# Optimization experiments

Measured on AMD Instinct MI355X. Metric: run time of the kernel, lower is better.

Reference implementation:

```python
import jax, jax.numpy as jnp
import numpy as np

B, A, C, H, W = 2, 4, 3, 32, 32
N = H * W * A  # 4096 proposals
EPS = 1e-6


def setup_inputs() -> dict:
    key = jax.random.key(0)
    k1, k2, k3, k4 = jax.random.split(key, 4)
    scores = jax.random.normal(k1, (B, A * C, H, W), jnp.float32)
    bbox_preds = jax.random.normal(k2, (B, A * 7, H, W), jnp.float32)
    pp_params = jax.random.normal(k3, (B, C * 3, H, W), jnp.float32)
    # decoded LiDAR boxes (x, y, z, dx, dy, dz, yaw) with positive sizes
    u = jax.random.uniform(k4, (B, N, 7), jnp.float32)
    scale = jnp.array([80.0, 80.0, 4.0, 4.0, 4.0, 3.0, 6.28], jnp.float32)
    shift = jnp.array([-40.0, -40.0, -2.0, 0.5, 0.5, 0.5, -3.14], jnp.float32)
    decoded = u * scale + shift
    return {"scores": scores, "bbox_preds": bbox_preds,
            "pp_params": pp_params, "decoded": decoded}


def _nearest_bev(dec):
    # dec: [B, N, 7] -> axis-aligned nearest BEV boxes [B, N, 4] (x1,y1,x2,y2)
    bev = dec[..., jnp.array([0, 1, 3, 4, 6])]  # x, y, dx, dy, yaw
    rot = bev[..., 4]
    period = jnp.pi
    # limit_period(rot, offset=0.5, period=pi)
    normed = jnp.abs(rot - jnp.floor(rot / period + 0.5) * period)
    cond = (normed > jnp.pi / 4)[..., None]
    xywh = jnp.where(cond, bev[..., jnp.array([0, 1, 3, 2])], bev[..., :4])
    ctr, dims = xywh[..., :2], xywh[..., 2:]
    return jnp.concatenate([ctr - dims / 2, ctr + dims / 2], axis=-1)


def _pairwise_iou(boxes):
    # boxes: [B, N, 4] -> iou [B, N, N]
    lt = jnp.maximum(boxes[:, :, None, :2], boxes[:, None, :, :2])
    rb = jnp.minimum(boxes[:, :, None, 2:], boxes[:, None, :, 2:])
    wh = jnp.clip(rb - lt, 0.0)
    inter = wh[..., 0] * wh[..., 1]
    area = (boxes[..., 2] - boxes[..., 0]) * (boxes[..., 3] - boxes[..., 1])
    union = area[:, :, None] + area[:, None, :] - inter
    return inter / jnp.maximum(union, EPS)


def _forward_scores(scores, pp_params, decoded):
    # flatten scores: [B, A*C, H, W] -> [B, N, C]
    sc = scores.reshape(B, A, C, H, W).transpose(0, 3, 4, 1, 2).reshape(B, N, C)
    # flatten pp: [B, C*3, H, W] -> [B, H, W, C, 3] -> expand over A -> [B, N, C, 3]
    pp = pp_params.reshape(B, C, 3, H, W).transpose(0, 3, 4, 1, 2)
    pp = jnp.broadcast_to(pp[:, :, :, None], (B, H, W, A, C, 3)).reshape(B, N, C, 3)

    iou = _pairwise_iou(_nearest_bev(decoded[..., :7]))  # [B, N, N]
    sm_sc = jax.nn.softmax(sc, axis=1)  # softmax over proposal dim per class

    per_class = []
    for c in range(C):  # C is small and fixed
        p0 = pp[:, :, c, 0]
        p1 = pp[:, :, c, 1]
        weight = jax.nn.softmax(iou + p0[:, :, None] * p1[:, None, :], axis=2)
        per_class.append(jnp.einsum('bij,bj->bi', weight, sm_sc[:, :, c]))
    new_sc = jnp.stack(per_class, axis=-1)  # [B, N, C]

    # back to level layout: [B, N, C] -> [B, A*C, H, W]
    return new_sc.reshape(B, H, W, A, C).transpose(0, 3, 4, 1, 2).reshape(B, A * C, H, W)


def reference(scores, bbox_preds, pp_params, decoded):
    out_scores = _forward_scores(scores, pp_params, decoded)
    # original returns (out_scores_list, bbox_preds, dir_cls, pp_params); dir_cls=None
    return out_scores, bbox_preds, pp_params
```

## Files before the change

kernel.cpp:

```cpp
#include <hip/hip_runtime.h>
#include <math.h>

#define B_   2
#define C_   3
#define HW_  1024
#define N_   4096
#define AC_  12

#define PI_F    3.14159265358979323846f
#define L2E     1.4426950408889634f
#define INV_L2E 0.6931471805599453f

#define OUT0_ELEMS 24576
#define OUT1_ELEMS 57344
#define OUT2_ELEMS 18432

#define ROWBLK   16
#define JTILE    512
#define NTILE    8
#define MAINBLKS 512
#define CPBLKS   32
#define CP_F4_BBOX 14336
#define CP_F4_TOT  18944

#if __has_builtin(__builtin_amdgcn_exp2f)
#define EXP2F(x) __builtin_amdgcn_exp2f(x)
#else
#define EXP2F(x) __expf((x) * INV_L2E)
#endif

__device__ __forceinline__ float4 make_box(const float* __restrict__ d) {
    float x = d[0], y = d[1], d3 = d[3], d4 = d[4], rot = d[6];
    float kq = floorf(rot / PI_F + 0.5f);
    float normed = fabsf(rot - kq * PI_F);
    bool swap_wh = normed > (0.25f * PI_F);
    float w = swap_wh ? d4 : d3;
    float h = swap_wh ? d3 : d4;
    return make_float4(x - 0.5f * w, y - 0.5f * h, x + 0.5f * w, y + 0.5f * h);
}

__global__ __launch_bounds__(512) void k_fused(
    const float* __restrict__ scores, const float* __restrict__ pp,
    const float* __restrict__ dec, const float* __restrict__ bbox,
    float* __restrict__ out)
{
    const int blk = blockIdx.x;
    const int t = threadIdx.x;

    if (blk >= MAINBLKS) {
        const float4* src1 = (const float4*)bbox;
        const float4* src2 = (const float4*)pp;
        float4* dst1 = (float4*)(out + OUT0_ELEMS);
        float4* dst2 = (float4*)(out + OUT0_ELEMS + OUT1_ELEMS);
        for (int u = (blk - MAINBLKS) * 512 + t; u < CP_F4_TOT;
             u += CPBLKS * 512) {
            if (u < CP_F4_BBOX) dst1[u] = src1[u];
            else                dst2[u - CP_F4_BBOX] = src2[u - CP_F4_BBOX];
        }
        return;
    }

    const int b = blk >> 8;
    const int rowblk = blk & 255;
    const int r = t & 15;
    const int q = t >> 4;

    const float* __restrict__ decb = dec + b * (N_ * 7);
    const float* __restrict__ scb  = scores + b * (AC_ * HW_);
    const float* __restrict__ ppb  = pp + b * (9 * HW_);

    __shared__ float4 s_box[JTILE];
    __shared__ float4 s_aux[JTILE];
    __shared__ float4 s_p1[JTILE];
    __shared__ float2 s_red[8][ROWBLK][C_];
    __shared__ float  s_Sp[8][C_];

    const int i0 = rowblk * ROWBLK + r;
    const float4 bx0 = make_box(decb + i0 * 7);
    const float ar0 = (bx0.z - bx0.x) * (bx0.w - bx0.y) * INV_L2E;
    const int hw0 = i0 >> 2;
    const float p00x = ppb[0 * HW_ + hw0] * L2E;
    const float p00y = ppb[3 * HW_ + hw0] * L2E;
    const float p00z = ppb[6 * HW_ + hw0] * L2E;

    float n00 = 0.f, d00 = 0.f, n01 = 0.f, d01 = 0.f, n02 = 0.f, d02 = 0.f;
    float sS0 = 0.f, sS1 = 0.f, sS2 = 0.f;

    float ld0, ld1, ld3, ld4, ld6, ls0, ls1, ls2, lp1a, lp1b, lp1c;
    {
        const float* dj = decb + t * 7;
        ld0 = dj[0]; ld1 = dj[1]; ld3 = dj[3]; ld4 = dj[4]; ld6 = dj[6];
        const int hw = t >> 2, a = t & 3;
        ls0 = scb[(a * C_ + 0) * HW_ + hw];
        ls1 = scb[(a * C_ + 1) * HW_ + hw];
        ls2 = scb[(a * C_ + 2) * HW_ + hw];
        lp1a = ppb[1 * HW_ + hw]; lp1b = ppb[4 * HW_ + hw]; lp1c = ppb[7 * HW_ + hw];
    }

    for (int tile = 0; tile < NTILE; ++tile) {
        if (tile) __syncthreads();
        {
            float kq = floorf(ld6 / PI_F + 0.5f);
            float normed = fabsf(ld6 - kq * PI_F);
            bool sw = normed > (0.25f * PI_F);
            float w = sw ? ld4 : ld3, h = sw ? ld3 : ld4;
            float4 box = make_float4(ld0 - 0.5f * w, ld1 - 0.5f * h,
                                     ld0 + 0.5f * w, ld1 + 0.5f * h);
            float area = (box.z - box.x) * (box.w - box.y);
            float e0 = __expf(ls0), e1 = __expf(ls1), e2 = __expf(ls2);
            sS0 += e0; sS1 += e1; sS2 += e2;
            s_box[t] = box;
            s_aux[t] = make_float4(area * INV_L2E, e0, e1, e2);
            s_p1[t]  = make_float4(lp1a, lp1b, lp1c, 0.f);
        }
        __syncthreads();
        if (tile + 1 < NTILE) {
            const int j = (tile + 1) * JTILE + t;
            const float* dj = decb + j * 7;
            ld0 = dj[0]; ld1 = dj[1]; ld3 = dj[3]; ld4 = dj[4]; ld6 = dj[6];
            const int hw = j >> 2, a = j & 3;
            ls0 = scb[(a * C_ + 0) * HW_ + hw];
            ls1 = scb[(a * C_ + 1) * HW_ + hw];
            ls2 = scb[(a * C_ + 2) * HW_ + hw];
            lp1a = ppb[1 * HW_ + hw]; lp1b = ppb[4 * HW_ + hw]; lp1c = ppb[7 * HW_ + hw];
        }
#pragma unroll 4
        for (int m = 0; m < 16; ++m) {
            const int jj = q + (m << 5);
            const float4 bj = s_box[jj];
            const float4 ax = s_aux[jj];
            const float4 pj = s_p1[jj];
            float x1 = fmaxf(bx0.x, bj.x), y1 = fmaxf(bx0.y, bj.y);
            float x2 = fminf(bx0.z, bj.z), y2 = fminf(bx0.w, bj.w);
            float w = fmaxf(x2 - x1, 0.f), h = fmaxf(y2 - y1, 0.f);
            float inter = w * h;
            float uni = fmaf(inter, -INV_L2E, ar0 + ax.x);
            float iou = inter * __builtin_amdgcn_rcpf(uni);
            float e0 = EXP2F(fmaf(p00x, pj.x, iou));
            float e1 = EXP2F(fmaf(p00y, pj.y, iou));
            float e2 = EXP2F(fmaf(p00z, pj.z, iou));
            n00 = fmaf(e0, ax.y, n00); d00 += e0;
            n01 = fmaf(e1, ax.z, n01); d01 += e1;
            n02 = fmaf(e2, ax.w, n02); d02 += e2;
        }
    }

#define RED4(v) { v += __shfl_xor(v, 16); v += __shfl_xor(v, 32); }
    RED4(n00) RED4(d00) RED4(n01) RED4(d01) RED4(n02) RED4(d02)
#undef RED4
    const int wv = t >> 6, lane = t & 63;
    if (lane < ROWBLK) {
        s_red[wv][lane][0] = make_float2(n00, d00);
        s_red[wv][lane][1] = make_float2(n01, d01);
        s_red[wv][lane][2] = make_float2(n02, d02);
    }
#pragma unroll
    for (int off = 1; off < 64; off <<= 1) {
        sS0 += __shfl_xor(sS0, off);
        sS1 += __shfl_xor(sS1, off);
        sS2 += __shfl_xor(sS2, off);
    }
    if (lane == 0) { s_Sp[wv][0] = sS0; s_Sp[wv][1] = sS1; s_Sp[wv][2] = sS2; }
    __syncthreads();

    if (t < C_ * ROWBLK) {
        const int c = t >> 4, row = t & 15;
        float num = 0.f, den = 0.f, S = 0.f;
#pragma unroll
        for (int w = 0; w < 8; ++w) {
            float2 v = s_red[w][row][c];
            num += v.x; den += v.y;
            S += s_Sp[w][c];
        }
        const int n = rowblk * ROWBLK + row;
        out[(b * AC_ + (n & 3) * C_ + c) * HW_ + (n >> 2)] = num / (den * S);
    }
}

extern "C" void kernel_launch(void* const* d_in, const int* in_sizes, int n_in,
                              void* d_out, int out_size, void* d_ws, size_t ws_size,
                              hipStream_t stream) {
    (void)d_ws; (void)ws_size;
    const float* scores = (const float*)d_in[0];
    const float* bbox   = (const float*)d_in[1];
    const float* pp     = (const float*)d_in[2];
    const float* dec    = (const float*)d_in[3];
    k_fused<<<MAINBLKS + CPBLKS, 512, 0, stream>>>(
        scores, pp, dec, bbox, (float*)d_out);
}
```

Before: 93.97 us.

## Register-block four rows per thread and double-buffer shared tiles

Each thread now handles four consecutive rows (the four anchors that share one hw position and its pp values), so every column entry read from shared memory is reused four times. The shared staging arrays are double-buffered, which allows the next tile to be written while the current one is consumed and removes one barrier per tile. Launch bounds now request 4 blocks per CU. The change cuts LDS traffic and barriers but raises register pressure and lengthens the shuffle reduction.

Measured after the change: 96.97 us. +3.2%, slower.

```diff
diff --git a/kernel.cpp b/kernel.cpp
--- a/kernel.cpp
+++ b/kernel.cpp
@@ -16,6 +16,7 @@
 #define OUT2_ELEMS 18432
 
 #define ROWBLK   16
+#define RPT      4
 #define JTILE    512
 #define NTILE    8
 #define MAINBLKS 512
@@ -39,7 +40,7 @@
     return make_float4(x - 0.5f * w, y - 0.5f * h, x + 0.5f * w, y + 0.5f * h);
 }
 
-__global__ __launch_bounds__(512) void k_fused(
+__global__ __launch_bounds__(512, 4) void k_fused(
     const float* __restrict__ scores, const float* __restrict__ pp,
     const float* __restrict__ dec, const float* __restrict__ bbox,
     float* __restrict__ out)
@@ -62,31 +63,36 @@
 
     const int b = blk >> 8;
     const int rowblk = blk & 255;
-    const int r = t & 15;
-    const int q = t >> 4;
+    const int r = t & 3;
+    const int q = t >> 2;
 
     const float* __restrict__ decb = dec + b * (N_ * 7);
     const float* __restrict__ scb  = scores + b * (AC_ * HW_);
     const float* __restrict__ ppb  = pp + b * (9 * HW_);
 
-    __shared__ float4 s_box[JTILE];
-    __shared__ float4 s_aux[JTILE];
-    __shared__ float4 s_p1[JTILE];
+    __shared__ float4 s_box[2][JTILE];
+    __shared__ float4 s_aux[2][JTILE];
+    __shared__ float4 s_p1 [2][JTILE];
     __shared__ float2 s_red[8][ROWBLK][C_];
     __shared__ float  s_Sp[8][C_];
 
-    const int i0 = rowblk * ROWBLK + r;
-    const float4 bx0 = make_box(decb + i0 * 7);
-    const float ar0 = (bx0.z - bx0.x) * (bx0.w - bx0.y) * INV_L2E;
+    const int i0 = rowblk * ROWBLK + (r << 2);
     const int hw0 = i0 >> 2;
-    const float p00x = ppb[0 * HW_ + hw0] * L2E;
-    const float p00y = ppb[3 * HW_ + hw0] * L2E;
-    const float p00z = ppb[6 * HW_ + hw0] * L2E;
-
-    float n00 = 0.f, d00 = 0.f, n01 = 0.f, d01 = 0.f, n02 = 0.f, d02 = 0.f;
+    float4 bx[RPT]; float ar[RPT];
+#pragma unroll
+    for (int k = 0; k < RPT; ++k) {
+        bx[k] = make_box(decb + (i0 + k) * 7);
+        ar[k] = (bx[k].z - bx[k].x) * (bx[k].w - bx[k].y) * INV_L2E;
+    }
+    const float p0x = ppb[0 * HW_ + hw0] * L2E;
+    const float p0y = ppb[3 * HW_ + hw0] * L2E;
+    const float p0z = ppb[6 * HW_ + hw0] * L2E;
+
+    float accn[RPT][C_] = {}, accd[RPT][C_] = {};
     float sS0 = 0.f, sS1 = 0.f, sS2 = 0.f;
 
     float ld0, ld1, ld3, ld4, ld6, ls0, ls1, ls2, lp1a, lp1b, lp1c;
+
     {
         const float* dj = decb + t * 7;
         ld0 = dj[0]; ld1 = dj[1]; ld3 = dj[3]; ld4 = dj[4]; ld6 = dj[6];
@@ -95,25 +101,24 @@
         ls1 = scb[(a * C_ + 1) * HW_ + hw];
         ls2 = scb[(a * C_ + 2) * HW_ + hw];
         lp1a = ppb[1 * HW_ + hw]; lp1b = ppb[4 * HW_ + hw]; lp1c = ppb[7 * HW_ + hw];
-    }
-
+        float kq = floorf(ld6 / PI_F + 0.5f);
+        float nr = fabsf(ld6 - kq * PI_F);
+        bool sw = nr > (0.25f * PI_F);
+        float w = sw ? ld4 : ld3, h = sw ? ld3 : ld4;
+        float4 box = make_float4(ld0 - 0.5f * w, ld1 - 0.5f * h,
+                                 ld0 + 0.5f * w, ld1 + 0.5f * h);
+        float area = (box.z - box.x) * (box.w - box.y);
+        float e0 = __expf(ls0), e1 = __expf(ls1), e2 = __expf(ls2);
+        sS0 += e0; sS1 += e1; sS2 += e2;
+        s_box[0][t] = box;
+        s_aux[0][t] = make_float4(area * INV_L2E, e0, e1, e2);
+        s_p1 [0][t] = make_float4(lp1a, lp1b, lp1c, 0.f);
+    }
+    __syncthreads();
+
+#pragma unroll 1
     for (int tile = 0; tile < NTILE; ++tile) {
-        if (tile) __syncthreads();
-        {
-            float kq = floorf(ld6 / PI_F + 0.5f);
-            float normed = fabsf(ld6 - kq * PI_F);
-            bool sw = normed > (0.25f * PI_F);
-            float w = sw ? ld4 : ld3, h = sw ? ld3 : ld4;
-            float4 box = make_float4(ld0 - 0.5f * w, ld1 - 0.5f * h,
-                                     ld0 + 0.5f * w, ld1 + 0.5f * h);
-            float area = (box.z - box.x) * (box.w - box.y);
-            float e0 = __expf(ls0), e1 = __expf(ls1), e2 = __expf(ls2);
-            sS0 += e0; sS1 += e1; sS2 += e2;
-            s_box[t] = box;
-            s_aux[t] = make_float4(area * INV_L2E, e0, e1, e2);
-            s_p1[t]  = make_float4(lp1a, lp1b, lp1c, 0.f);
-        }
-        __syncthreads();
+        const int cur = tile & 1;
         if (tile + 1 < NTILE) {
             const int j = (tile + 1) * JTILE + t;
             const float* dj = decb + j * 7;
@@ -124,35 +129,65 @@
             ls2 = scb[(a * C_ + 2) * HW_ + hw];
             lp1a = ppb[1 * HW_ + hw]; lp1b = ppb[4 * HW_ + hw]; lp1c = ppb[7 * HW_ + hw];
         }
-#pragma unroll 4
-        for (int m = 0; m < 16; ++m) {
-            const int jj = q + (m << 5);
-            const float4 bj = s_box[jj];
-            const float4 ax = s_aux[jj];
-            const float4 pj = s_p1[jj];
-            float x1 = fmaxf(bx0.x, bj.x), y1 = fmaxf(bx0.y, bj.y);
-            float x2 = fminf(bx0.z, bj.z), y2 = fminf(bx0.w, bj.w);
-            float w = fmaxf(x2 - x1, 0.f), h = fmaxf(y2 - y1, 0.f);
-            float inter = w * h;
-            float uni = fmaf(inter, -INV_L2E, ar0 + ax.x);
-            float iou = inter * __builtin_amdgcn_rcpf(uni);
-            float e0 = EXP2F(fmaf(p00x, pj.x, iou));
-            float e1 = EXP2F(fmaf(p00y, pj.y, iou));
-            float e2 = EXP2F(fmaf(p00z, pj.z, iou));
-            n00 = fmaf(e0, ax.y, n00); d00 += e0;
-            n01 = fmaf(e1, ax.z, n01); d01 += e1;
-            n02 = fmaf(e2, ax.w, n02); d02 += e2;
-        }
-    }
-
-#define RED4(v) { v += __shfl_xor(v, 16); v += __shfl_xor(v, 32); }
-    RED4(n00) RED4(d00) RED4(n01) RED4(d01) RED4(n02) RED4(d02)
-#undef RED4
+#pragma unroll 2
+        for (int m = 0; m < JTILE / 128; ++m) {
+            const int jj = q + (m << 7);
+            const float4 bj = s_box[cur][jj];
+            const float4 ax = s_aux[cur][jj];
+            const float4 pj = s_p1 [cur][jj];
+#pragma unroll
+            for (int k = 0; k < RPT; ++k) {
+                float x1 = fmaxf(bx[k].x, bj.x), y1 = fmaxf(bx[k].y, bj.y);
+                float x2 = fminf(bx[k].z, bj.z), y2 = fminf(bx[k].w, bj.w);
+                float w = fmaxf(x2 - x1, 0.f), h = fmaxf(y2 - y1, 0.f);
+                float inter = w * h;
+                float uni = fmaf(inter, -INV_L2E, ar[k] + ax.x);
+                float iou = inter * __builtin_amdgcn_rcpf(uni);
+                float e0 = EXP2F(fmaf(p0x, pj.x, iou));
+                float e1 = EXP2F(fmaf(p0y, pj.y, iou));
+                float e2 = EXP2F(fmaf(p0z, pj.z, iou));
+                accn[k][0] = fmaf(e0, ax.y, accn[k][0]); accd[k][0] += e0;
+                accn[k][1] = fmaf(e1, ax.z, accn[k][1]); accd[k][1] += e1;
+                accn[k][2] = fmaf(e2, ax.w, accn[k][2]); accd[k][2] += e2;
+            }
+        }
+        if (tile + 1 < NTILE) {
+            float kq = floorf(ld6 / PI_F + 0.5f);
+            float nr = fabsf(ld6 - kq * PI_F);
+            bool sw = nr > (0.25f * PI_F);
+            float w = sw ? ld4 : ld3, h = sw ? ld3 : ld4;
+            float4 box = make_float4(ld0 - 0.5f * w, ld1 - 0.5f * h,
+                                     ld0 + 0.5f * w, ld1 + 0.5f * h);
+            float area = (box.z - box.x) * (box.w - box.y);
+            float e0 = __expf(ls0), e1 = __expf(ls1), e2 = __expf(ls2);
+            sS0 += e0; sS1 += e1; sS2 += e2;
+            const int nxt = cur ^ 1;
+            s_box[nxt][t] = box;
+            s_aux[nxt][t] = make_float4(area * INV_L2E, e0, e1, e2);
+            s_p1 [nxt][t] = make_float4(lp1a, lp1b, lp1c, 0.f);
+        }
+        __syncthreads();
+    }
+
+#pragma unroll
+    for (int k = 0; k < RPT; ++k)
+#pragma unroll
+        for (int c = 0; c < C_; ++c) {
+            float nv = accn[k][c], dv = accd[k][c];
+            nv += __shfl_xor(nv, 4);  dv += __shfl_xor(dv, 4);
+            nv += __shfl_xor(nv, 8);  dv += __shfl_xor(dv, 8);
+            nv += __shfl_xor(nv, 16); dv += __shfl_xor(dv, 16);
+            nv += __shfl_xor(nv, 32); dv += __shfl_xor(dv, 32);
+            accn[k][c] = nv; accd[k][c] = dv;
+        }
     const int wv = t >> 6, lane = t & 63;
-    if (lane < ROWBLK) {
-        s_red[wv][lane][0] = make_float2(n00, d00);
-        s_red[wv][lane][1] = make_float2(n01, d01);
-        s_red[wv][lane][2] = make_float2(n02, d02);
+    if (lane < 4) {
+#pragma unroll
+        for (int k = 0; k < RPT; ++k)
+#pragma unroll
+            for (int c = 0; c < C_; ++c)
+                s_red[wv][(lane << 2) + k][c] =
+                    make_float2(accn[k][c], accd[k][c]);
     }
 #pragma unroll
     for (int off = 1; off < 64; off <<= 1) {
```

## Factor pp term out of exp across anchor groups and compute two rows per thread

Applied to the files above, without the earlier changes.

Splits exp(iou + p0*p1) into exp(iou)*exp(p0*p1). The p1 value is shared by the 4 anchors at each spatial location, so the per-class exp is computed once per location rather than once per proposal, and only one exp(iou) is needed per pair instead of three. Each thread now handles two rows, sharing the shared-memory loads of column boxes and halving the number of blocks, which lowers parallelism. The factored exponentials can overflow or lose precision if the two terms are large with opposite signs.

Measured after the change: 85.64 us. 8.9% less time.

```diff
diff --git a/kernel.cpp b/kernel.cpp
--- a/kernel.cpp
+++ b/kernel.cpp
@@ -15,10 +15,11 @@
 #define OUT1_ELEMS 57344
 #define OUT2_ELEMS 18432
 
-#define ROWBLK   16
+#define ROWBLK   32
 #define JTILE    512
+#define QTILE    128
 #define NTILE    8
-#define MAINBLKS 512
+#define MAINBLKS 256
 #define CPBLKS   32
 #define CP_F4_BBOX 14336
 #define CP_F4_TOT  18944
@@ -60,8 +61,8 @@
         return;
     }
 
-    const int b = blk >> 8;
-    const int rowblk = blk & 255;
+    const int b = blk >> 7;
+    const int rowblk = blk & 127;
     const int r = t & 15;
     const int q = t >> 4;
 
@@ -71,22 +72,24 @@
 
     __shared__ float4 s_box[JTILE];
     __shared__ float4 s_aux[JTILE];
-    __shared__ float4 s_p1[JTILE];
+    __shared__ float4 s_p1q[QTILE];
     __shared__ float2 s_red[8][ROWBLK][C_];
     __shared__ float  s_Sp[8][C_];
 
-    const int i0 = rowblk * ROWBLK + r;
+    const int i0 = rowblk * ROWBLK + (r << 1);
     const float4 bx0 = make_box(decb + i0 * 7);
+    const float4 bx1 = make_box(decb + (i0 + 1) * 7);
     const float ar0 = (bx0.z - bx0.x) * (bx0.w - bx0.y) * INV_L2E;
+    const float ar1 = (bx1.z - bx1.x) * (bx1.w - bx1.y) * INV_L2E;
     const int hw0 = i0 >> 2;
-    const float p00x = ppb[0 * HW_ + hw0] * L2E;
-    const float p00y = ppb[3 * HW_ + hw0] * L2E;
-    const float p00z = ppb[6 * HW_ + hw0] * L2E;
-
-    float n00 = 0.f, d00 = 0.f, n01 = 0.f, d01 = 0.f, n02 = 0.f, d02 = 0.f;
+    const float p0x = ppb[0 * HW_ + hw0] * L2E;
+    const float p0y = ppb[3 * HW_ + hw0] * L2E;
+    const float p0z = ppb[6 * HW_ + hw0] * L2E;
+
+    float accn[2][C_] = {}, accd[2][C_] = {};
     float sS0 = 0.f, sS1 = 0.f, sS2 = 0.f;
 
-    float ld0, ld1, ld3, ld4, ld6, ls0, ls1, ls2, lp1a, lp1b, lp1c;
+    float ld0, ld1, ld3, ld4, ld6, ls0, ls1, ls2, lq1a = 0.f, lq1b = 0.f, lq1c = 0.f;
     {
         const float* dj = decb + t * 7;
         ld0 = dj[0]; ld1 = dj[1]; ld3 = dj[3]; ld4 = dj[4]; ld6 = dj[6];
@@ -94,15 +97,17 @@
         ls0 = scb[(a * C_ + 0) * HW_ + hw];
         ls1 = scb[(a * C_ + 1) * HW_ + hw];
         ls2 = scb[(a * C_ + 2) * HW_ + hw];
-        lp1a = ppb[1 * HW_ + hw]; lp1b = ppb[4 * HW_ + hw]; lp1c = ppb[7 * HW_ + hw];
+        if (t < QTILE) {
+            lq1a = ppb[1 * HW_ + t]; lq1b = ppb[4 * HW_ + t]; lq1c = ppb[7 * HW_ + t];
+        }
     }
 
     for (int tile = 0; tile < NTILE; ++tile) {
         if (tile) __syncthreads();
         {
             float kq = floorf(ld6 / PI_F + 0.5f);
-            float normed = fabsf(ld6 - kq * PI_F);
-            bool sw = normed > (0.25f * PI_F);
+            float nr = fabsf(ld6 - kq * PI_F);
+            bool sw = nr > (0.25f * PI_F);
             float w = sw ? ld4 : ld3, h = sw ? ld3 : ld4;
             float4 box = make_float4(ld0 - 0.5f * w, ld1 - 0.5f * h,
                                      ld0 + 0.5f * w, ld1 + 0.5f * h);
@@ -111,7 +116,7 @@
             sS0 += e0; sS1 += e1; sS2 += e2;
             s_box[t] = box;
             s_aux[t] = make_float4(area * INV_L2E, e0, e1, e2);
-            s_p1[t]  = make_float4(lp1a, lp1b, lp1c, 0.f);
+            if (t < QTILE) s_p1q[t] = make_float4(lq1a, lq1b, lq1c, 0.f);
         }
         __syncthreads();
         if (tile + 1 < NTILE) {
@@ -122,38 +127,76 @@
             ls0 = scb[(a * C_ + 0) * HW_ + hw];
             ls1 = scb[(a * C_ + 1) * HW_ + hw];
             ls2 = scb[(a * C_ + 2) * HW_ + hw];
-            lp1a = ppb[1 * HW_ + hw]; lp1b = ppb[4 * HW_ + hw]; lp1c = ppb[7 * HW_ + hw];
-        }
-#pragma unroll 4
-        for (int m = 0; m < 16; ++m) {
-            const int jj = q + (m << 5);
-            const float4 bj = s_box[jj];
-            const float4 ax = s_aux[jj];
-            const float4 pj = s_p1[jj];
-            float x1 = fmaxf(bx0.x, bj.x), y1 = fmaxf(bx0.y, bj.y);
-            float x2 = fminf(bx0.z, bj.z), y2 = fminf(bx0.w, bj.w);
-            float w = fmaxf(x2 - x1, 0.f), h = fmaxf(y2 - y1, 0.f);
-            float inter = w * h;
-            float uni = fmaf(inter, -INV_L2E, ar0 + ax.x);
-            float iou = inter * __builtin_amdgcn_rcpf(uni);
-            float e0 = EXP2F(fmaf(p00x, pj.x, iou));
-            float e1 = EXP2F(fmaf(p00y, pj.y, iou));
-            float e2 = EXP2F(fmaf(p00z, pj.z, iou));
-            n00 = fmaf(e0, ax.y, n00); d00 += e0;
-            n01 = fmaf(e1, ax.z, n01); d01 += e1;
-            n02 = fmaf(e2, ax.w, n02); d02 += e2;
-        }
-    }
-
-#define RED4(v) { v += __shfl_xor(v, 16); v += __shfl_xor(v, 32); }
-    RED4(n00) RED4(d00) RED4(n01) RED4(d01) RED4(n02) RED4(d02)
-#undef RED4
+            if (t < QTILE) {
+                const int uq = (tile + 1) * QTILE + t;
+                lq1a = ppb[1 * HW_ + uq]; lq1b = ppb[4 * HW_ + uq]; lq1c = ppb[7 * HW_ + uq];
+            }
+        }
+#pragma unroll
+        for (int mm = 0; mm < QTILE / 32; ++mm) {
+            const int u = q + (mm << 5);
+            const float4 pq = s_p1q[u];
+            const float g0 = EXP2F(p0x * pq.x);
+            const float g1 = EXP2F(p0y * pq.y);
+            const float g2 = EXP2F(p0z * pq.z);
+            float Eq0 = 0.f, Eq1 = 0.f;
+            float t00 = 0.f, t01 = 0.f, t02 = 0.f;
+            float t10 = 0.f, t11 = 0.f, t12 = 0.f;
+#pragma unroll
+            for (int js = 0; js < 4; ++js) {
+                const int jj = (u << 2) + js;
+                const float4 bj = s_box[jj];
+                const float4 ax = s_aux[jj];
+                {
+                    float x1 = fmaxf(bx0.x, bj.x), y1 = fmaxf(bx0.y, bj.y);
+                    float x2 = fminf(bx0.z, bj.z), y2 = fminf(bx0.w, bj.w);
+                    float w = fmaxf(x2 - x1, 0.f), h = fmaxf(y2 - y1, 0.f);
+                    float inter = w * h;
+                    float uni = fmaf(inter, -INV_L2E, ar0 + ax.x);
+                    float E = EXP2F(inter * __builtin_amdgcn_rcpf(uni));
+                    Eq0 += E;
+                    t00 = fmaf(E, ax.y, t00);
+                    t01 = fmaf(E, ax.z, t01);
+                    t02 = fmaf(E, ax.w, t02);
+                }
+                {
+                    float x1 = fmaxf(bx1.x, bj.x), y1 = fmaxf(bx1.y, bj.y);
+                    float x2 = fminf(bx1.z, bj.z), y2 = fminf(bx1.w, bj.w);
+                    float w = fmaxf(x2 - x1, 0.f), h = fmaxf(y2 - y1, 0.f);
+                    float inter = w * h;
+                    float uni = fmaf(inter, -INV_L2E, ar1 + ax.x);
+                    float E = EXP2F(inter * __builtin_amdgcn_rcpf(uni));
+                    Eq1 += E;
+                    t10 = fmaf(E, ax.y, t10);
+                    t11 = fmaf(E, ax.z, t11);
+                    t12 = fmaf(E, ax.w, t12);
+                }
+            }
+            accd[0][0] = fmaf(g0, Eq0, accd[0][0]);
+            accd[0][1] = fmaf(g1, Eq0, accd[0][1]);
+            accd[0][2] = fmaf(g2, Eq0, accd[0][2]);
+            accn[0][0] = fmaf(g0, t00, accn[0][0]);
+            accn[0][1] = fmaf(g1, t01, accn[0][1]);
+            accn[0][2] = fmaf(g2, t02, accn[0][2]);
+            accd[1][0] = fmaf(g0, Eq1, accd[1][0]);
+            accd[1][1] = fmaf(g1, Eq1, accd[1][1]);
+            accd[1][2] = fmaf(g2, Eq1, accd[1][2]);
+            accn[1][0] = fmaf(g0, t10, accn[1][0]);
+            accn[1][1] = fmaf(g1, t11, accn[1][1]);
+            accn[1][2] = fmaf(g2, t12, accn[1][2]);
+        }
+    }
+
     const int wv = t >> 6, lane = t & 63;
-    if (lane < ROWBLK) {
-        s_red[wv][lane][0] = make_float2(n00, d00);
-        s_red[wv][lane][1] = make_float2(n01, d01);
-        s_red[wv][lane][2] = make_float2(n02, d02);
-    }
+#pragma unroll
+    for (int k = 0; k < 2; ++k)
+#pragma unroll
+        for (int c = 0; c < C_; ++c) {
+            float nv = accn[k][c], dv = accd[k][c];
+            nv += __shfl_xor(nv, 16); dv += __shfl_xor(dv, 16);
+            nv += __shfl_xor(nv, 32); dv += __shfl_xor(dv, 32);
+            if (lane < 16) s_red[wv][(lane << 1) + k][c] = make_float2(nv, dv);
+        }
 #pragma unroll
     for (int off = 1; off < 64; off <<= 1) {
         sS0 += __shfl_xor(sS0, off);
@@ -164,7 +207,7 @@
     __syncthreads();
 
     if (t < C_ * ROWBLK) {
-        const int c = t >> 4, row = t & 15;
+        const int c = t >> 5, row = t & 31;
         float num = 0.f, den = 0.f, S = 0.f;
 #pragma unroll
         for (int w = 0; w < 8; ++w) {
```
